# Optimization experiments

Measured on AMD Instinct MI355X. Metric: run time of the kernel, lower is better.

## Reference

```python
import jax, jax.numpy as jnp
import numpy as np

B, L, D, C, DEPTH = 2, 1024, 256, 16, 4
N = L // C  # chunks per sequence
EPS = 1.1920929e-07  # torch RMSNorm default eps = finfo(fp32).eps


def rmsnorm(x, w):
    return x * jax.lax.rsqrt(jnp.mean(x * x, axis=-1, keepdims=True) + EPS) * w


def mlp_apply(ws, x):
    # titans MLP: x @ W0, then silu -> @ W1, ... (works for batched [*,d,d] weights too)
    for i, w in enumerate(ws):
        if i:
            x = jax.nn.silu(x)
        x = x @ w
    return x


def setup_inputs() -> dict:
    key = jax.random.key(0)
    ks = jax.random.split(key, 10)
    s = np.float32(1.0 / np.sqrt(D))
    return {
        "seq": jax.random.normal(ks[0], (B, L, D), jnp.float32),
        "w_store_norm": jnp.ones((D,), jnp.float32),
        "w_retrieve_norm": jnp.ones((D,), jnp.float32),
        "w_post_norm": jnp.ones((D,), jnp.float32),
        "Wq": jax.random.normal(ks[1], (D, D), jnp.float32) * s,
        "Wkv": jax.random.normal(ks[2], (D, 2 * D), jnp.float32) * s,
        "w_adapt": jax.random.normal(ks[3], (D,), jnp.float32) * s,
        "w_mom": jax.random.normal(ks[4], (D,), jnp.float32) * s,
        "w_decay": jax.random.normal(ks[5], (D,), jnp.float32) * s,
        "W0": jax.random.normal(ks[6], (D, D), jnp.float32) * s,
        "W1": jax.random.normal(ks[7], (D, D), jnp.float32) * s,
        "W2": jax.random.normal(ks[8], (D, D), jnp.float32) * s,
        "W3": jax.random.normal(ks[9], (D, D), jnp.float32) * s,
    }


def _forward(seq, w_store_norm, w_retrieve_norm, w_post_norm, Wq, Wkv,
             w_adapt, w_mom, w_decay, W0, W1, W2, W3):
    ws = (W0, W1, W2, W3)

    # ---------------- store_memories ----------------
    sn = rmsnorm(seq, w_store_norm)                      # [B,L,D]; L already multiple of C
    cm = sn.reshape(B, N, C, D).mean(axis=2)             # per-chunk mean [B,N,D]
    adaptive_lr = jax.nn.sigmoid(cm @ w_adapt)           # [B,N]
    adaptive_mom = jax.nn.sigmoid(cm @ w_mom)[..., None]   # [B,N,1]
    decay = jax.nn.sigmoid(cm @ w_decay)[..., None]        # [B,N,1]

    kv = sn @ Wkv                                        # [B,L,2D]
    keys = kv[..., :D].reshape(B * N, C, D)
    vals = kv[..., D:].reshape(B * N, C, D)

    def chunk_loss(params, k, v):
        pred = mlp_apply(params, k)                      # [C,D]
        return jnp.sum(jnp.mean((pred - v) ** 2, axis=-1))

    # per-chunk grads wrt the 4 MLP weights (past weights are zero at init)
    grads = jax.vmap(jax.grad(chunk_loss), in_axes=(None, 0, 0))(ws, keys, vals)
    g = jnp.stack(grads, axis=1).reshape(B, N, DEPTH * D * D)  # packed 'b n *'
    surprise = -adaptive_lr[..., None] * g               # [B,N,P]

    def op(l, r):
        al, xl = l
        ar, xr = r
        return (al * ar, xl * ar + xr)                   # x_t = a_t*x_{t-1} + b_t

    _, momentum = jax.lax.associative_scan(op, (adaptive_mom, surprise), axis=1)
    _, updates = jax.lax.associative_scan(op, (1.0 - decay, momentum), axis=1)
    upd = updates.reshape(B, N, DEPTH, D, D)

    # per-chunk fast weights: base params + cumulative update
    fast_ws = tuple((w + upd[:, :, i]).reshape(B * N, D, D) for i, w in enumerate(ws))

    # ---------------- retrieve_memories ----------------
    rn = rmsnorm(seq, w_retrieve_norm)[:, C - 1:]        # [B, L-C+1, D]
    rn = jnp.pad(rn, ((0, 0), (0, C - 1), (0, 0)))       # pad back up to [B,L,D]
    q = (rn @ Wq).reshape(B * N, C, D)
    out = mlp_apply(fast_ws, q).reshape(B, L, D)         # batched fast-weight MLP
    out = rmsnorm(out, w_post_norm)
    out = jnp.pad(out, ((0, 0), (C - 1, 0), (0, 0)))[:, :-(C - 1)]  # shift by C-1
    return out


def reference(seq, w_store_norm, w_retrieve_norm, w_post_norm, Wq, Wkv,
              w_adapt, w_mom, w_decay, W0, W1, W2, W3):
    return _forward(seq, w_store_norm, w_retrieve_norm, w_post_norm, Wq, Wkv,
                    w_adapt, w_mom, w_decay, W0, W1, W2, W3)
```

## Files before the change

kernel.cpp:

```cpp
#include <hip/hip_runtime.h>
#include <hip/hip_bf16.h>

typedef __attribute__((ext_vector_type(8)))  short s8v;
typedef __attribute__((ext_vector_type(4)))  float f4v;
typedef _Float16 h4 __attribute__((ext_vector_type(4)));
typedef __attribute__((ext_vector_type(4))) unsigned short u4v;

constexpr int NCn  = 128;
constexpr int DDn  = 65536;
constexpr int XP   = 264;
constexpr float EPSf = 1.1920929e-07f;

__device__ __forceinline__ float sigm(float x){ return 1.0f/(1.0f + expf(-x)); }
__device__ __forceinline__ float silu_(float x){ return x * sigm(x); }
__device__ __forceinline__ float dsilu_(float x){ float s = sigm(x); return s*(1.0f + x*(1.0f - s)); }

__device__ __forceinline__ unsigned short f2b(float x){
    __hip_bfloat16 b = __float2bfloat16(x);
    unsigned short u; __builtin_memcpy(&u, &b, 2); return u;
}
__device__ __forceinline__ float b2f(unsigned short u){
    __hip_bfloat16 b; __builtin_memcpy(&b, &u, 2); return __bfloat162float(b);
}
__device__ __forceinline__ h4 ldh4(const unsigned short* p){
    h4 r; __builtin_memcpy(&r, p, 8); return r;
}

__device__ __forceinline__ int fidx(int row, int col){
    return (((row >> 4)*8 + (col >> 5))*4 + ((col >> 3) & 3))*128 + (row & 15)*8 + (col & 7);
}

__global__ __launch_bounds__(256) void ktw(const float* __restrict__ Wq,
        const float* __restrict__ Wkv, const float* __restrict__ W0,
        const float* __restrict__ W1, const float* __restrict__ W2,
        const float* __restrict__ W3, unsigned short* __restrict__ WTb,
        unsigned short* __restrict__ WqTb, unsigned short* __restrict__ WkvTb,
        unsigned short* __restrict__ Wb){
    int z = blockIdx.z;
    if (z >= 6){
        const float* S = (z==6)?W1:(z==7)?W2:W3;
        size_t idx = (((size_t)blockIdx.y*8 + blockIdx.x)*256 + threadIdx.x)*2;
        float2 v = *(const float2*)(S + idx);
        ushort2 u; u.x = f2b(v.x); u.y = f2b(v.y);
        int row = (int)(idx >> 8), col = (int)(idx & 255);
        *(ushort2*)(Wb + (size_t)(z-6)*DDn + fidx(row, col)) = u;
        return;
    }
    __shared__ float tl[32][33];
    if (z != 5 && blockIdx.y >= 8) return;
    const float* S; unsigned short* T; int C;
    if (z < 4){ S = (z==0)?W0:(z==1)?W1:(z==2)?W2:W3; T = WTb + (size_t)z*DDn; C = 256; }
    else if (z == 4){ S = Wq; T = WqTb; C = 256; }
    else { S = Wkv; T = WkvTb; C = 512; }
    int k0 = blockIdx.x*32, j0 = blockIdx.y*32;
    int tx = threadIdx.x & 31, ty = threadIdx.x >> 5;
    #pragma unroll
    for (int p = 0; p < 4; ++p)
        tl[ty + 8*p][tx] = S[(size_t)(k0 + ty + 8*p)*C + j0 + tx];
    __syncthreads();
    #pragma unroll
    for (int p = 0; p < 4; ++p){
        int r = j0 + ty + 8*p, k = k0 + tx;
        T[fidx(r, k)] = f2b(tl[tx][ty + 8*p]);
    }
}

__global__ __launch_bounds__(1024, 1) void kfb(const float* __restrict__ seq,
        const float* __restrict__ wsn,
        const unsigned short* __restrict__ WkvTb, const unsigned short* __restrict__ WTb,
        const unsigned short* __restrict__ Wb,
        const float* __restrict__ wa, const float* __restrict__ wm,
        const float* __restrict__ wdk,
        float* __restrict__ momg, float* __restrict__ decg,
        unsigned short* __restrict__ XT, unsigned short* __restrict__ GT){
    __shared__ unsigned short xs[16][XP];
    __shared__ unsigned short xl[4][16][XP];
    __shared__ unsigned short Gs[16][XP];
    __shared__ float red3[16][4];
    int tid = threadIdx.x, w = tid >> 6, lane = tid & 63;
    int m16 = lane & 15, q16 = lane >> 4;
    int g = blockIdx.x;
    int n0 = w*16;
    size_t fb = (size_t)w*4096 + q16*128 + m16*8;

    {
        const float4 xv = *(const float4*)(seq + ((size_t)g*16 + w)*256 + lane*4);
        const float4 wv = *(const float4*)(wsn + lane*4);
        float ssq = xv.x*xv.x + xv.y*xv.y + xv.z*xv.z + xv.w*xv.w;
        #pragma unroll
        for (int off = 32; off; off >>= 1) ssq += __shfl_xor(ssq, off, 64);
        float s2 = rsqrtf(ssq*(1.f/256.f) + EPSf);
        u4v sv;
        sv[0] = f2b(xv.x*s2*wv.x); sv[1] = f2b(xv.y*s2*wv.y);
        sv[2] = f2b(xv.z*s2*wv.z); sv[3] = f2b(xv.w*s2*wv.w);
        *(u4v*)(&xs[w][lane*4]) = sv;
    }
    __syncthreads();

    float sc;
    {
        int d2 = tid & 255, qt = tid >> 8;
        float a = 0.f;
        #pragma unroll
        for (int c = 0; c < 4; ++c)
            a += b2f(xs[qt*4 + c][d2]);
        float cm = a * (1.f/16.f);
        float s0 = cm*wa[d2], s1 = cm*wm[d2], s2 = cm*wdk[d2];
        #pragma unroll
        for (int off = 32; off; off >>= 1){
            s0 += __shfl_down(s0, off, 64);
            s1 += __shfl_down(s1, off, 64);
            s2 += __shfl_down(s2, off, 64);
        }
        if (lane == 0){ red3[w][0] = s0; red3[w][1] = s1; red3[w][2] = s2; }
        __syncthreads();
        float da = 0.f, dm = 0.f, dc = 0.f;
        #pragma unroll
        for (int i = 0; i < 16; ++i){
            da += red3[i][0]; dm += red3[i][1]; dc += red3[i][2];
        }
        sc = -2.f * sigm(da) * (1.f/256.f);
        if (tid == 0){ momg[g] = sigm(dm); decg[g] = sigm(dc); }
    }

    s8v af[8];
    #pragma unroll
    for (int i = 0; i < 8; ++i) af[i] = *(const s8v*)(&xs[m16][q16*8 + i*32]);

    s8v bpre[8];
    #pragma unroll
    for (int i = 0; i < 8; ++i) bpre[i] = *(const s8v*)(WTb + fb + i*512);

    f4v vacc;
    {
        f4v ka = {0.f,0.f,0.f,0.f}, va = {0.f,0.f,0.f,0.f};
        const unsigned short* brK = WkvTb + fb;
        const unsigned short* brV = WkvTb + (size_t)DDn + fb;
        #pragma unroll
        for (int i = 0; i < 8; ++i){
            s8v bK = *(const s8v*)(brK + i*512);
            s8v bV = *(const s8v*)(brV + i*512);
            ka = __builtin_amdgcn_mfma_f32_16x16x32_bf16(af[i], bK, ka, 0, 0, 0);
            va = __builtin_amdgcn_mfma_f32_16x16x32_bf16(af[i], bV, va, 0, 0, 0);
        }
        vacc = va;
        #pragma unroll
        for (int r = 0; r < 4; ++r) xl[0][4*q16 + r][n0 + m16] = f2b(ka[r]);
    }

    f4v hreg[3];
    #pragma unroll
    for (int l = 0; l < 3; ++l){
        __syncthreads();
        s8v xa[8];
        #pragma unroll
        for (int i = 0; i < 8; ++i)
            xa[i] = *(const s8v*)(&xl[l][m16][q16*8 + i*32]);
        s8v bcur[8];
        #pragma unroll
        for (int i = 0; i < 8; ++i) bcur[i] = bpre[i];
        const unsigned short* nxt = WTb + (size_t)(l+1)*DDn + fb;
        #pragma unroll
        for (int i = 0; i < 8; ++i) bpre[i] = *(const s8v*)(nxt + i*512);
        f4v acc = {0.f,0.f,0.f,0.f};
        #pragma unroll
        for (int i = 0; i < 8; ++i)
            acc = __builtin_amdgcn_mfma_f32_16x16x32_bf16(xa[i], bcur[i], acc, 0, 0, 0);
        hreg[l] = acc;
        #pragma unroll
        for (int r = 0; r < 4; ++r)
            xl[l+1][4*q16 + r][n0 + m16] = f2b(silu_(acc[r]));
    }
    __syncthreads();

    {
        int d = tid & 255, qt = tid >> 8;
        #pragma unroll
        for (int l = 0; l < 4; ++l){
            h4 v;
            #pragma unroll
            for (int j = 0; j < 4; ++j)
                v[j] = (_Float16)b2f(xl[l][qt*4 + j][d]);
            *(h4*)(XT + (((size_t)l*128 + g)*256 + d)*16 + qt*4) = v;
        }
    }

    {
        s8v xa[8];
        #pragma unroll
        for (int i = 0; i < 8; ++i)
            xa[i] = *(const s8v*)(&xl[3][m16][q16*8 + i*32]);
        s8v bcur[8];
        #pragma unroll
        for (int i = 0; i < 8; ++i) bcur[i] = bpre[i];
        const unsigned short* nxt = Wb + (size_t)2*DDn + fb;
        #pragma unroll
        for (int i = 0; i < 8; ++i) bpre[i] = *(const s8v*)(nxt + i*512);
        f4v acc = {0.f,0.f,0.f,0.f};
        #pragma unroll
        for (int i = 0; i < 8; ++i)
            acc = __builtin_amdgcn_mfma_f32_16x16x32_bf16(xa[i], bcur[i], acc, 0, 0, 0);
        #pragma unroll
        for (int r = 0; r < 4; ++r)
            Gs[4*q16 + r][n0 + m16] = f2b(sc * (acc[r] - vacc[r]));
    }
    __syncthreads();
    {
        int d = tid & 255, qt = tid >> 8;
        h4 v;
        #pragma unroll
        for (int j = 0; j < 4; ++j)
            v[j] = (_Float16)b2f(Gs[qt*4 + j][d]);
        *(h4*)(GT + (((size_t)3*128 + g)*256 + d)*16 + qt*4) = v;
    }

    #pragma unroll
    for (int l = 3; l >= 1; --l){
        s8v gfa[8];
        #pragma unroll
        for (int i = 0; i < 8; ++i)
            gfa[i] = *(const s8v*)(&Gs[m16][q16*8 + i*32]);
        s8v bcur[8];
        #pragma unroll
        for (int i = 0; i < 8; ++i) bcur[i] = bpre[i];
        if (l > 1){
            const unsigned short* nxt = Wb + (size_t)(l-2)*DDn + fb;
            #pragma unroll
            for (int i = 0; i < 8; ++i) bpre[i] = *(const s8v*)(nxt + i*512);
        }
        f4v acc = {0.f,0.f,0.f,0.f};
        #pragma unroll
        for (int i = 0; i < 8; ++i)
            acc = __builtin_amdgcn_mfma_f32_16x16x32_bf16(gfa[i], bcur[i], acc, 0, 0, 0);
        f4v gn;
        #pragma unroll
        for (int r = 0; r < 4; ++r)
            gn[r] = acc[r] * dsilu_(hreg[l-1][r]);
        __syncthreads();
        #pragma unroll
        for (int r = 0; r < 4; ++r)
            Gs[4*q16 + r][n0 + m16] = f2b(gn[r]);
        __syncthreads();
        {
            int d = tid & 255, qt = tid >> 8;
            h4 v;
            #pragma unroll
            for (int j = 0; j < 4; ++j)
                v[j] = (_Float16)b2f(Gs[qt*4 + j][d]);
            *(h4*)(GT + (((size_t)(l-1)*128 + g)*256 + d)*16 + qt*4) = v;
        }
    }
}

__global__ __launch_bounds__(64, 1) void kck(const unsigned short* __restrict__ XT,
        const unsigned short* __restrict__ GT, const float* __restrict__ momg,
        const float* __restrict__ decg, unsigned short* __restrict__ ucpb){
    __shared__ unsigned short ts[16][18];
    int lane = threadIdx.x;
    int m16 = lane & 15, q16 = lane >> 4;
    int rt = blockIdx.x, ct = blockIdx.y, bl = blockIdx.z;
    int b = bl >> 2, l = bl & 3;
    int dr = rt*16 + m16;
    const unsigned short* Gb = GT + ((size_t)l*128 + b*64)*4096 + (size_t)dr*16 + q16*4;
    const unsigned short* X0 = XT + ((size_t)l*128 + b*64)*4096
                             + (size_t)(ct*16 + m16)*16 + q16*4;
    int rr = lane & 15, cg = lane >> 4;
    int off0;
    {
        int c0 = ct*16 + cg*4;
        off0 = ((rt*8 + (c0 >> 5))*4 + ((c0 >> 3) & 3))*128 + rr*8 + (c0 & 7);
    }
    f4v us = {0.f,0.f,0.f,0.f}, ms = {0.f,0.f,0.f,0.f};
    #pragma unroll 4
    for (int n = 0; n < 64; ++n){
        float mo = momg[b*64 + n], de = 1.f - decg[b*64 + n];
        h4 a  = ldh4(Gb + (size_t)n*4096);
        h4 x0 = ldh4(X0 + (size_t)n*4096);
        f4v z = {0.f,0.f,0.f,0.f};
        f4v s = __builtin_amdgcn_mfma_f32_16x16x16f16(a, x0, z, 0, 0, 0);
        #pragma unroll
        for (int r = 0; r < 4; ++r){
            float mn = mo*ms[r] + s[r], un = de*us[r] + mn;
            ms[r] = mn; us[r] = un;
            ts[4*q16 + r][m16] = f2b(un);
        }
        size_t cb = ((size_t)bl*64 + n)*65536;
        u4v v0;
        #pragma unroll
        for (int j = 0; j < 4; ++j)
            v0[j] = ts[rr][cg*4 + j];
        *(u4v*)(ucpb + cb + off0) = v0;
    }
}

__global__ __launch_bounds__(1024, 1) void kretr(const float* __restrict__ seq,
        const float* __restrict__ wrn,
        const unsigned short* __restrict__ WqTb, const unsigned short* __restrict__ WTb,
        const unsigned short* __restrict__ ucpb, const float* __restrict__ wpost,
        float* __restrict__ out){
    __shared__ unsigned short xc[2][16][XP];
    __shared__ float red[16][16];
    __shared__ float rs[16];
    int tid = threadIdx.x, w = tid >> 6, lane = tid & 63;
    int m16 = lane & 15, q16 = lane >> 4;
    int g = blockIdx.x;
    int b = g >> 6, nl = g & 63;
    int n0 = w*16;
    size_t fb = (size_t)w*4096 + q16*128 + m16*8;
    const unsigned short* ubase = ucpb + ((size_t)(b*4)*64 + nl)*65536 + fb;

    s8v upre[8];
    #pragma unroll
    for (int i = 0; i < 8; ++i) upre[i] = *(const s8v*)(ubase + i*512);

    {
        int p = nl*16 + w + 15;
        u4v sv = {0,0,0,0};
        if (p < 1024){
            const float4 xv = *(const float4*)(seq + ((size_t)b*1024 + p)*256 + lane*4);
            const float4 wv = *(const float4*)(wrn + lane*4);
            float ssq = xv.x*xv.x + xv.y*xv.y + xv.z*xv.z + xv.w*xv.w;
            #pragma unroll
            for (int off = 32; off; off >>= 1) ssq += __shfl_xor(ssq, off, 64);
            float s2 = rsqrtf(ssq*(1.f/256.f) + EPSf);
            sv[0] = f2b(xv.x*s2*wv.x); sv[1] = f2b(xv.y*s2*wv.y);
            sv[2] = f2b(xv.z*s2*wv.z); sv[3] = f2b(xv.w*s2*wv.w);
        }
        *(u4v*)(&xc[1][w][lane*4]) = sv;
    }
    __syncthreads();

    {
        s8v a[8];
        #pragma unroll
        for (int i = 0; i < 8; ++i) a[i] = *(const s8v*)(&xc[1][m16][q16*8 + i*32]);
        f4v acc = {0.f,0.f,0.f,0.f};
        const unsigned short* br = WqTb + fb;
        #pragma unroll
        for (int i = 0; i < 8; ++i){
            s8v bb = *(const s8v*)(br + i*512);
            acc = __builtin_amdgcn_mfma_f32_16x16x32_bf16(a[i], bb, acc, 0, 0, 0);
        }
        #pragma unroll
        for (int r = 0; r < 4; ++r) xc[0][4*q16 + r][n0 + m16] = f2b(acc[r]);
    }
    __syncthreads();

    f4v hacc;
    for (int l = 0; l < 4; ++l){
        s8v xa[8];
        #pragma unroll
        for (int i = 0; i < 8; ++i)
            xa[i] = *(const s8v*)(&xc[l & 1][m16][q16*8 + i*32]);
        s8v ucur[8];
        #pragma unroll
        for (int i = 0; i < 8; ++i) ucur[i] = upre[i];
        if (l < 3){
            const unsigned short* un = ubase + (size_t)(l+1)*64*65536;
            #pragma unroll
            for (int i = 0; i < 8; ++i) upre[i] = *(const s8v*)(un + i*512);
        }
        const unsigned short* br = WTb + (size_t)l*DDn + fb;
        f4v aW = {0.f,0.f,0.f,0.f}, aU = {0.f,0.f,0.f,0.f};
        #pragma unroll
        for (int i = 0; i < 8; ++i){
            s8v w0 = *(const s8v*)(br + i*512);
            aW = __builtin_amdgcn_mfma_f32_16x16x32_bf16(xa[i], w0, aW, 0, 0, 0);
            aU = __builtin_amdgcn_mfma_f32_16x16x32_bf16(xa[i], ucur[i], aU, 0, 0, 0);
        }
        #pragma unroll
        for (int r = 0; r < 4; ++r) hacc[r] = aW[r] + aU[r];
        if (l < 3){
            #pragma unroll
            for (int r = 0; r < 4; ++r)
                xc[(l + 1) & 1][4*q16 + r][n0 + m16] = f2b(silu_(hacc[r]));
            __syncthreads();
        }
    }

    float part[4];
    #pragma unroll
    for (int r = 0; r < 4; ++r) part[r] = hacc[r]*hacc[r];
    #pragma unroll
    for (int off = 1; off < 16; off <<= 1)
        #pragma unroll
        for (int r = 0; r < 4; ++r) part[r] += __shfl_xor(part[r], off, 64);
    if (m16 == 0)
        #pragma unroll
        for (int r = 0; r < 4; ++r) red[w][4*q16 + r] = part[r];
    __syncthreads();
    if (tid < 16){
        float s = 0.f;
        #pragma unroll
        for (int i = 0; i < 16; ++i) s += red[i][tid];
        rs[tid] = rsqrtf(s*(1.f/256.f) + EPSf);
    }
    __syncthreads();
    {
        int d = n0 + m16;
        float wp = wpost[d];
        #pragma unroll
        for (int r = 0; r < 4; ++r){
            int c = 4*q16 + r;
            int tp = nl*16 + c + 15;
            if (tp < 1024)
                out[((size_t)b*1024 + tp)*256 + d] = hacc[r]*rs[c]*wp;
        }
    }
    if (nl == 0){
        for (int idx = tid; idx < 15*256; idx += 1024)
            out[(size_t)b*262144 + idx] = 0.f;
    }
}

extern "C" void kernel_launch(void* const* d_in, const int* in_sizes, int n_in,
                              void* d_out, int out_size, void* d_ws, size_t ws_size,
                              hipStream_t stream) {
    const float* seq     = (const float*)d_in[0];
    const float* w_store = (const float*)d_in[1];
    const float* w_retr  = (const float*)d_in[2];
    const float* w_post  = (const float*)d_in[3];
    const float* Wq      = (const float*)d_in[4];
    const float* Wkv     = (const float*)d_in[5];
    const float* w_adapt = (const float*)d_in[6];
    const float* w_mom   = (const float*)d_in[7];
    const float* w_decay = (const float*)d_in[8];
    const float* W0      = (const float*)d_in[9];
    const float* W1      = (const float*)d_in[10];
    const float* W2      = (const float*)d_in[11];
    const float* W3      = (const float*)d_in[12];

    float* momg  = (float*)d_ws;
    float* decg  = momg + NCn;
    unsigned short* WTb   = (unsigned short*)(decg + NCn + 32);
    unsigned short* Wb    = WTb   + 4*(size_t)DDn;
    unsigned short* WqTb  = Wb    + 3*(size_t)DDn;
    unsigned short* WkvTb = WqTb  + (size_t)DDn;
    unsigned short* XT    = WkvTb + 2*(size_t)DDn;
    unsigned short* GT    = XT    + (size_t)4*NCn*4096;
    unsigned short* ucpb  = GT    + (size_t)4*NCn*4096;

    ktw   <<<dim3(8, 16, 9),  256,  0, stream>>>(Wq, Wkv, W0, W1, W2, W3,
                                                 WTb, WqTb, WkvTb, Wb);
    kfb   <<<dim3(NCn),       1024, 0, stream>>>(seq, w_store, WkvTb, WTb, Wb,
                                                 w_adapt, w_mom, w_decay,
                                                 momg, decg, XT, GT);
    kck   <<<dim3(16, 16, 8), 64,   0, stream>>>(XT, GT, momg, decg, ucpb);
    kretr <<<dim3(NCn),       1024, 0, stream>>>(seq, w_retr, WqTb, WTb, ucpb,
                                                 w_post, (float*)d_out);
}
```

Before: 138.1 us.

## Fuse forward, chunk-scan and retrieval kernels into one cooperative kernel

Merges the three kernels kfb, kck and kretr into a single cooperative kernel with 128 blocks of 1024 threads, separated by grid-wide syncs. The scan phase is remapped so that each of the 16 waves per block handles one of the former 64-thread kck blocks. This removes two kernel launch boundaries and their inter-kernel gaps. In exchange it adds the cost of grid barriers and the cooperative-launch overhead, and it places all the phases' shared memory in one block, which could limit scheduling.

```diff
diff --git a/kernel.cpp b/kernel.cpp
--- a/kernel.cpp
+++ b/kernel.cpp
@@ -1,5 +1,8 @@
 #include <hip/hip_runtime.h>
 #include <hip/hip_bf16.h>
+#include <hip/hip_cooperative_groups.h>
+
+namespace cg = cooperative_groups;
 
 typedef __attribute__((ext_vector_type(8)))  short s8v;
 typedef __attribute__((ext_vector_type(4)))  float f4v;
@@ -65,18 +68,25 @@
     }
 }
 
-__global__ __launch_bounds__(1024, 1) void kfb(const float* __restrict__ seq,
-        const float* __restrict__ wsn,
+__global__ __launch_bounds__(1024, 1) void kmain(const float* __restrict__ seq,
+        const float* __restrict__ wsn, const float* __restrict__ wrn,
         const unsigned short* __restrict__ WkvTb, const unsigned short* __restrict__ WTb,
-        const unsigned short* __restrict__ Wb,
+        const unsigned short* __restrict__ Wb, const unsigned short* __restrict__ WqTb,
         const float* __restrict__ wa, const float* __restrict__ wm,
         const float* __restrict__ wdk,
         float* __restrict__ momg, float* __restrict__ decg,
-        unsigned short* __restrict__ XT, unsigned short* __restrict__ GT){
+        unsigned short* __restrict__ XT, unsigned short* __restrict__ GT,
+        unsigned short* __restrict__ ucpb,
+        const float* __restrict__ wpost, float* __restrict__ out){
     __shared__ unsigned short xs[16][XP];
     __shared__ unsigned short xl[4][16][XP];
     __shared__ unsigned short Gs[16][XP];
     __shared__ float red3[16][4];
+    __shared__ unsigned short ts[16][16][18];
+    __shared__ unsigned short xc[2][16][XP];
+    __shared__ float red[16][16];
+    __shared__ float rs[16];
+
     int tid = threadIdx.x, w = tid >> 6, lane = tid & 63;
     int m16 = lane & 15, q16 = lane >> 4;
     int g = blockIdx.x;
@@ -84,162 +94,127 @@
     size_t fb = (size_t)w*4096 + q16*128 + m16*8;
 
     {
-        const float4 xv = *(const float4*)(seq + ((size_t)g*16 + w)*256 + lane*4);
-        const float4 wv = *(const float4*)(wsn + lane*4);
-        float ssq = xv.x*xv.x + xv.y*xv.y + xv.z*xv.z + xv.w*xv.w;
-        #pragma unroll
-        for (int off = 32; off; off >>= 1) ssq += __shfl_xor(ssq, off, 64);
-        float s2 = rsqrtf(ssq*(1.f/256.f) + EPSf);
-        u4v sv;
-        sv[0] = f2b(xv.x*s2*wv.x); sv[1] = f2b(xv.y*s2*wv.y);
-        sv[2] = f2b(xv.z*s2*wv.z); sv[3] = f2b(xv.w*s2*wv.w);
-        *(u4v*)(&xs[w][lane*4]) = sv;
-    }
-    __syncthreads();
-
-    float sc;
-    {
-        int d2 = tid & 255, qt = tid >> 8;
-        float a = 0.f;
-        #pragma unroll
-        for (int c = 0; c < 4; ++c)
-            a += b2f(xs[qt*4 + c][d2]);
-        float cm = a * (1.f/16.f);
-        float s0 = cm*wa[d2], s1 = cm*wm[d2], s2 = cm*wdk[d2];
-        #pragma unroll
-        for (int off = 32; off; off >>= 1){
-            s0 += __shfl_down(s0, off, 64);
-            s1 += __shfl_down(s1, off, 64);
-            s2 += __shfl_down(s2, off, 64);
-        }
-        if (lane == 0){ red3[w][0] = s0; red3[w][1] = s1; red3[w][2] = s2; }
-        __syncthreads();
-        float da = 0.f, dm = 0.f, dc = 0.f;
-        #pragma unroll
-        for (int i = 0; i < 16; ++i){
-            da += red3[i][0]; dm += red3[i][1]; dc += red3[i][2];
-        }
-        sc = -2.f * sigm(da) * (1.f/256.f);
-        if (tid == 0){ momg[g] = sigm(dm); decg[g] = sigm(dc); }
-    }
-
-    s8v af[8];
-    #pragma unroll
-    for (int i = 0; i < 8; ++i) af[i] = *(const s8v*)(&xs[m16][q16*8 + i*32]);
-
-    s8v bpre[8];
-    #pragma unroll
-    for (int i = 0; i < 8; ++i) bpre[i] = *(const s8v*)(WTb + fb + i*512);
-
-    f4v vacc;
-    {
-        f4v ka = {0.f,0.f,0.f,0.f}, va = {0.f,0.f,0.f,0.f};
-        const unsigned short* brK = WkvTb + fb;
-        const unsigned short* brV = WkvTb + (size_t)DDn + fb;
-        #pragma unroll
-        for (int i = 0; i < 8; ++i){
-            s8v bK = *(const s8v*)(brK + i*512);
-            s8v bV = *(const s8v*)(brV + i*512);
-            ka = __builtin_amdgcn_mfma_f32_16x16x32_bf16(af[i], bK, ka, 0, 0, 0);
-            va = __builtin_amdgcn_mfma_f32_16x16x32_bf16(af[i], bV, va, 0, 0, 0);
-        }
-        vacc = va;
-        #pragma unroll
-        for (int r = 0; r < 4; ++r) xl[0][4*q16 + r][n0 + m16] = f2b(ka[r]);
-    }
-
-    f4v hreg[3];
-    #pragma unroll
-    for (int l = 0; l < 3; ++l){
-        __syncthreads();
-        s8v xa[8];
-        #pragma unroll
-        for (int i = 0; i < 8; ++i)
-            xa[i] = *(const s8v*)(&xl[l][m16][q16*8 + i*32]);
-        s8v bcur[8];
-        #pragma unroll
-        for (int i = 0; i < 8; ++i) bcur[i] = bpre[i];
-        const unsigned short* nxt = WTb + (size_t)(l+1)*DDn + fb;
-        #pragma unroll
-        for (int i = 0; i < 8; ++i) bpre[i] = *(const s8v*)(nxt + i*512);
-        f4v acc = {0.f,0.f,0.f,0.f};
-        #pragma unroll
-        for (int i = 0; i < 8; ++i)
-            acc = __builtin_amdgcn_mfma_f32_16x16x32_bf16(xa[i], bcur[i], acc, 0, 0, 0);
-        hreg[l] = acc;
-        #pragma unroll
-        for (int r = 0; r < 4; ++r)
-            xl[l+1][4*q16 + r][n0 + m16] = f2b(silu_(acc[r]));
-    }
-    __syncthreads();
-
-    {
-        int d = tid & 255, qt = tid >> 8;
-        #pragma unroll
-        for (int l = 0; l < 4; ++l){
-            h4 v;
-            #pragma unroll
-            for (int j = 0; j < 4; ++j)
-                v[j] = (_Float16)b2f(xl[l][qt*4 + j][d]);
-            *(h4*)(XT + (((size_t)l*128 + g)*256 + d)*16 + qt*4) = v;
-        }
-    }
-
-    {
-        s8v xa[8];
-        #pragma unroll
-        for (int i = 0; i < 8; ++i)
-            xa[i] = *(const s8v*)(&xl[3][m16][q16*8 + i*32]);
-        s8v bcur[8];
-        #pragma unroll
-        for (int i = 0; i < 8; ++i) bcur[i] = bpre[i];
-        const unsigned short* nxt = Wb + (size_t)2*DDn + fb;
-        #pragma unroll
-        for (int i = 0; i < 8; ++i) bpre[i] = *(const s8v*)(nxt + i*512);
-        f4v acc = {0.f,0.f,0.f,0.f};
-        #pragma unroll
-        for (int i = 0; i < 8; ++i)
-            acc = __builtin_amdgcn_mfma_f32_16x16x32_bf16(xa[i], bcur[i], acc, 0, 0, 0);
-        #pragma unroll
-        for (int r = 0; r < 4; ++r)
-            Gs[4*q16 + r][n0 + m16] = f2b(sc * (acc[r] - vacc[r]));
-    }
-    __syncthreads();
-    {
-        int d = tid & 255, qt = tid >> 8;
-        h4 v;
-        #pragma unroll
-        for (int j = 0; j < 4; ++j)
-            v[j] = (_Float16)b2f(Gs[qt*4 + j][d]);
-        *(h4*)(GT + (((size_t)3*128 + g)*256 + d)*16 + qt*4) = v;
-    }
-
-    #pragma unroll
-    for (int l = 3; l >= 1; --l){
-        s8v gfa[8];
-        #pragma unroll
-        for (int i = 0; i < 8; ++i)
-            gfa[i] = *(const s8v*)(&Gs[m16][q16*8 + i*32]);
-        s8v bcur[8];
-        #pragma unroll
-        for (int i = 0; i < 8; ++i) bcur[i] = bpre[i];
-        if (l > 1){
-            const unsigned short* nxt = Wb + (size_t)(l-2)*DDn + fb;
+        {
+            const float4 xv = *(const float4*)(seq + ((size_t)g*16 + w)*256 + lane*4);
+            const float4 wv = *(const float4*)(wsn + lane*4);
+            float ssq = xv.x*xv.x + xv.y*xv.y + xv.z*xv.z + xv.w*xv.w;
+            #pragma unroll
+            for (int off = 32; off; off >>= 1) ssq += __shfl_xor(ssq, off, 64);
+            float s2 = rsqrtf(ssq*(1.f/256.f) + EPSf);
+            u4v sv;
+            sv[0] = f2b(xv.x*s2*wv.x); sv[1] = f2b(xv.y*s2*wv.y);
+            sv[2] = f2b(xv.z*s2*wv.z); sv[3] = f2b(xv.w*s2*wv.w);
+            *(u4v*)(&xs[w][lane*4]) = sv;
+        }
+        __syncthreads();
+
+        float sc;
+        {
+            int d2 = tid & 255, qt = tid >> 8;
+            float a = 0.f;
+            #pragma unroll
+            for (int c = 0; c < 4; ++c)
+                a += b2f(xs[qt*4 + c][d2]);
+            float cm = a * (1.f/16.f);
+            float s0 = cm*wa[d2], s1 = cm*wm[d2], s2 = cm*wdk[d2];
+            #pragma unroll
+            for (int off = 32; off; off >>= 1){
+                s0 += __shfl_down(s0, off, 64);
+                s1 += __shfl_down(s1, off, 64);
+                s2 += __shfl_down(s2, off, 64);
+            }
+            if (lane == 0){ red3[w][0] = s0; red3[w][1] = s1; red3[w][2] = s2; }
+            __syncthreads();
+            float da = 0.f, dm = 0.f, dc = 0.f;
+            #pragma unroll
+            for (int i = 0; i < 16; ++i){
+                da += red3[i][0]; dm += red3[i][1]; dc += red3[i][2];
+            }
+            sc = -2.f * sigm(da) * (1.f/256.f);
+            if (tid == 0){ momg[g] = sigm(dm); decg[g] = sigm(dc); }
+        }
+
+        s8v af[8];
+        #pragma unroll
+        for (int i = 0; i < 8; ++i) af[i] = *(const s8v*)(&xs[m16][q16*8 + i*32]);
+
+        s8v bpre[8];
+        #pragma unroll
+        for (int i = 0; i < 8; ++i) bpre[i] = *(const s8v*)(WTb + fb + i*512);
+
+        f4v vacc;
+        {
+            f4v ka = {0.f,0.f,0.f,0.f}, va = {0.f,0.f,0.f,0.f};
+            const unsigned short* brK = WkvTb + fb;
+            const unsigned short* brV = WkvTb + (size_t)DDn + fb;
+            #pragma unroll
+            for (int i = 0; i < 8; ++i){
+                s8v bK = *(const s8v*)(brK + i*512);
+                s8v bV = *(const s8v*)(brV + i*512);
+                ka = __builtin_amdgcn_mfma_f32_16x16x32_bf16(af[i], bK, ka, 0, 0, 0);
+                va = __builtin_amdgcn_mfma_f32_16x16x32_bf16(af[i], bV, va, 0, 0, 0);
+            }
+            vacc = va;
+            #pragma unroll
+            for (int r = 0; r < 4; ++r) xl[0][4*q16 + r][n0 + m16] = f2b(ka[r]);
+        }
+
+        f4v hreg[3];
+        #pragma unroll
+        for (int l = 0; l < 3; ++l){
+            __syncthreads();
+            s8v xa[8];
+            #pragma unroll
+            for (int i = 0; i < 8; ++i)
+                xa[i] = *(const s8v*)(&xl[l][m16][q16*8 + i*32]);
+            s8v bcur[8];
+            #pragma unroll
+            for (int i = 0; i < 8; ++i) bcur[i] = bpre[i];
+            const unsigned short* nxt = WTb + (size_t)(l+1)*DDn + fb;
             #pragma unroll
             for (int i = 0; i < 8; ++i) bpre[i] = *(const s8v*)(nxt + i*512);
-        }
-        f4v acc = {0.f,0.f,0.f,0.f};
-        #pragma unroll
-        for (int i = 0; i < 8; ++i)
-            acc = __builtin_amdgcn_mfma_f32_16x16x32_bf16(gfa[i], bcur[i], acc, 0, 0, 0);
-        f4v gn;
-        #pragma unroll
-        for (int r = 0; r < 4; ++r)
-            gn[r] = acc[r] * dsilu_(hreg[l-1][r]);
-        __syncthreads();
-        #pragma unroll
-        for (int r = 0; r < 4; ++r)
-            Gs[4*q16 + r][n0 + m16] = f2b(gn[r]);
+            f4v acc = {0.f,0.f,0.f,0.f};
+            #pragma unroll
+            for (int i = 0; i < 8; ++i)
+                acc = __builtin_amdgcn_mfma_f32_16x16x32_bf16(xa[i], bcur[i], acc, 0, 0, 0);
+            hreg[l] = acc;
+            #pragma unroll
+            for (int r = 0; r < 4; ++r)
+                xl[l+1][4*q16 + r][n0 + m16] = f2b(silu_(acc[r]));
+        }
+        __syncthreads();
+
+        {
+            int d = tid & 255, qt = tid >> 8;
+            #pragma unroll
+            for (int l = 0; l < 4; ++l){
+                h4 v;
+                #pragma unroll
+                for (int j = 0; j < 4; ++j)
+                    v[j] = (_Float16)b2f(xl[l][qt*4 + j][d]);
+                *(h4*)(XT + (((size_t)l*128 + g)*256 + d)*16 + qt*4) = v;
+            }
+        }
+
+        {
+            s8v xa[8];
+            #pragma unroll
+            for (int i = 0; i < 8; ++i)
+                xa[i] = *(const s8v*)(&xl[3][m16][q16*8 + i*32]);
+            s8v bcur[8];
+            #pragma unroll
+            for (int i = 0; i < 8; ++i) bcur[i] = bpre[i];
+            const unsigned short* nxt = Wb + (size_t)2*DDn + fb;
+            #pragma unroll
+            for (int i = 0; i < 8; ++i) bpre[i] = *(const s8v*)(nxt + i*512);
+            f4v acc = {0.f,0.f,0.f,0.f};
+            #pragma unroll
+            for (int i = 0; i < 8; ++i)
+                acc = __builtin_amdgcn_mfma_f32_16x16x32_bf16(xa[i], bcur[i], acc, 0, 0, 0);
+            #pragma unroll
+            for (int r = 0; r < 4; ++r)
+                Gs[4*q16 + r][n0 + m16] = f2b(sc * (acc[r] - vacc[r]));
+        }
         __syncthreads();
         {
             int d = tid & 255, qt = tid >> 8;
@@ -247,169 +222,194 @@
             #pragma unroll
             for (int j = 0; j < 4; ++j)
                 v[j] = (_Float16)b2f(Gs[qt*4 + j][d]);
-            *(h4*)(GT + (((size_t)(l-1)*128 + g)*256 + d)*16 + qt*4) = v;
+            *(h4*)(GT + (((size_t)3*128 + g)*256 + d)*16 + qt*4) = v;
+        }
+
+        #pragma unroll
+        for (int l = 3; l >= 1; --l){
+            s8v gfa[8];
+            #pragma unroll
+            for (int i = 0; i < 8; ++i)
+                gfa[i] = *(const s8v*)(&Gs[m16][q16*8 + i*32]);
+            s8v bcur[8];
+            #pragma unroll
+            for (int i = 0; i < 8; ++i) bcur[i] = bpre[i];
+            if (l > 1){
+                const unsigned short* nxt = Wb + (size_t)(l-2)*DDn + fb;
+                #pragma unroll
+                for (int i = 0; i < 8; ++i) bpre[i] = *(const s8v*)(nxt + i*512);
+            }
+            f4v acc = {0.f,0.f,0.f,0.f};
+            #pragma unroll
+            for (int i = 0; i < 8; ++i)
+                acc = __builtin_amdgcn_mfma_f32_16x16x32_bf16(gfa[i], bcur[i], acc, 0, 0, 0);
+            f4v gn;
+            #pragma unroll
+            for (int r = 0; r < 4; ++r)
+                gn[r] = acc[r] * dsilu_(hreg[l-1][r]);
+            __syncthreads();
+            #pragma unroll
+            for (int r = 0; r < 4; ++r)
+                Gs[4*q16 + r][n0 + m16] = f2b(gn[r]);
+            __syncthreads();
+            {
+                int d = tid & 255, qt = tid >> 8;
+                h4 v;
+                #pragma unroll
+                for (int j = 0; j < 4; ++j)
+                    v[j] = (_Float16)b2f(Gs[qt*4 + j][d]);
+                *(h4*)(GT + (((size_t)(l-1)*128 + g)*256 + d)*16 + qt*4) = v;
+            }
         }
     }
-}
-
-__global__ __launch_bounds__(64, 1) void kck(const unsigned short* __restrict__ XT,
-        const unsigned short* __restrict__ GT, const float* __restrict__ momg,
-        const float* __restrict__ decg, unsigned short* __restrict__ ucpb){
-    __shared__ unsigned short ts[16][18];
-    int lane = threadIdx.x;
-    int m16 = lane & 15, q16 = lane >> 4;
-    int rt = blockIdx.x, ct = blockIdx.y, bl = blockIdx.z;
-    int b = bl >> 2, l = bl & 3;
-    int dr = rt*16 + m16;
-    const unsigned short* Gb = GT + ((size_t)l*128 + b*64)*4096 + (size_t)dr*16 + q16*4;
-    const unsigned short* X0 = XT + ((size_t)l*128 + b*64)*4096
-                             + (size_t)(ct*16 + m16)*16 + q16*4;
-    int rr = lane & 15, cg = lane >> 4;
-    int off0;
+
+    cg::this_grid().sync();
+
     {
-        int c0 = ct*16 + cg*4;
-        off0 = ((rt*8 + (c0 >> 5))*4 + ((c0 >> 3) & 3))*128 + rr*8 + (c0 & 7);
+        int W = g*16 + w;
+        int rt = W >> 7, ct = (W >> 3) & 15, bl = W & 7;
+        int b = bl >> 2, l = bl & 3;
+        int dr = rt*16 + m16;
+        const unsigned short* Gb = GT + ((size_t)l*128 + b*64)*4096 + (size_t)dr*16 + q16*4;
+        const unsigned short* X0 = XT + ((size_t)l*128 + b*64)*4096
+                                 + (size_t)(ct*16 + m16)*16 + q16*4;
+        int rr = lane & 15, cg2 = lane >> 4;
+        int off0;
+        {
+            int c0 = ct*16 + cg2*4;
+            off0 = ((rt*8 + (c0 >> 5))*4 + ((c0 >> 3) & 3))*128 + rr*8 + (c0 & 7);
+        }
+        f4v us = {0.f,0.f,0.f,0.f}, ms = {0.f,0.f,0.f,0.f};
+        #pragma unroll 4
+        for (int n = 0; n < 64; ++n){
+            float mo = momg[b*64 + n], de = 1.f - decg[b*64 + n];
+            h4 a  = ldh4(Gb + (size_t)n*4096);
+            h4 x0 = ldh4(X0 + (size_t)n*4096);
+            f4v z = {0.f,0.f,0.f,0.f};
+            f4v s = __builtin_amdgcn_mfma_f32_16x16x16f16(a, x0, z, 0, 0, 0);
+            #pragma unroll
+            for (int r = 0; r < 4; ++r){
+                float mn = mo*ms[r] + s[r], un = de*us[r] + mn;
+                ms[r] = mn; us[r] = un;
+                ts[w][4*q16 + r][m16] = f2b(un);
+            }
+            size_t cb = ((size_t)bl*64 + n)*65536;
+            u4v v0;
+            #pragma unroll
+            for (int j = 0; j < 4; ++j)
+                v0[j] = ts[w][rr][cg2*4 + j];
+            *(u4v*)(ucpb + cb + off0) = v0;
+        }
     }
-    f4v us = {0.f,0.f,0.f,0.f}, ms = {0.f,0.f,0.f,0.f};
-    #pragma unroll 4
-    for (int n = 0; n < 64; ++n){
-        float mo = momg[b*64 + n], de = 1.f - decg[b*64 + n];
-        h4 a  = ldh4(Gb + (size_t)n*4096);
-        h4 x0 = ldh4(X0 + (size_t)n*4096);
-        f4v z = {0.f,0.f,0.f,0.f};
-        f4v s = __builtin_amdgcn_mfma_f32_16x16x16f16(a, x0, z, 0, 0, 0);
-        #pragma unroll
-        for (int r = 0; r < 4; ++r){
-            float mn = mo*ms[r] + s[r], un = de*us[r] + mn;
-            ms[r] = mn; us[r] = un;
-            ts[4*q16 + r][m16] = f2b(un);
-        }
-        size_t cb = ((size_t)bl*64 + n)*65536;
-        u4v v0;
-        #pragma unroll
-        for (int j = 0; j < 4; ++j)
-            v0[j] = ts[rr][cg*4 + j];
-        *(u4v*)(ucpb + cb + off0) = v0;
-    }
-}
-
-__global__ __launch_bounds__(1024, 1) void kretr(const float* __restrict__ seq,
-        const float* __restrict__ wrn,
-        const unsigned short* __restrict__ WqTb, const unsigned short* __restrict__ WTb,
-        const unsigned short* __restrict__ ucpb, const float* __restrict__ wpost,
-        float* __restrict__ out){
-    __shared__ unsigned short xc[2][16][XP];
-    __shared__ float red[16][16];
-    __shared__ float rs[16];
-    int tid = threadIdx.x, w = tid >> 6, lane = tid & 63;
-    int m16 = lane & 15, q16 = lane >> 4;
-    int g = blockIdx.x;
-    int b = g >> 6, nl = g & 63;
-    int n0 = w*16;
-    size_t fb = (size_t)w*4096 + q16*128 + m16*8;
-    const unsigned short* ubase = ucpb + ((size_t)(b*4)*64 + nl)*65536 + fb;
-
-    s8v upre[8];
-    #pragma unroll
-    for (int i = 0; i < 8; ++i) upre[i] = *(const s8v*)(ubase + i*512);
+
+    cg::this_grid().sync();
 
     {
-        int p = nl*16 + w + 15;
-        u4v sv = {0,0,0,0};
-        if (p < 1024){
-            const float4 xv = *(const float4*)(seq + ((size_t)b*1024 + p)*256 + lane*4);
-            const float4 wv = *(const float4*)(wrn + lane*4);
-            float ssq = xv.x*xv.x + xv.y*xv.y + xv.z*xv.z + xv.w*xv.w;
-            #pragma unroll
-            for (int off = 32; off; off >>= 1) ssq += __shfl_xor(ssq, off, 64);
-            float s2 = rsqrtf(ssq*(1.f/256.f) + EPSf);
-            sv[0] = f2b(xv.x*s2*wv.x); sv[1] = f2b(xv.y*s2*wv.y);
-            sv[2] = f2b(xv.z*s2*wv.z); sv[3] = f2b(xv.w*s2*wv.w);
-        }
-        *(u4v*)(&xc[1][w][lane*4]) = sv;
-    }
-    __syncthreads();
-
-    {
-        s8v a[8];
-        #pragma unroll
-        for (int i = 0; i < 8; ++i) a[i] = *(const s8v*)(&xc[1][m16][q16*8 + i*32]);
-        f4v acc = {0.f,0.f,0.f,0.f};
-        const unsigned short* br = WqTb + fb;
-        #pragma unroll
-        for (int i = 0; i < 8; ++i){
-            s8v bb = *(const s8v*)(br + i*512);
-            acc = __builtin_amdgcn_mfma_f32_16x16x32_bf16(a[i], bb, acc, 0, 0, 0);
-        }
-        #pragma unroll
-        for (int r = 0; r < 4; ++r) xc[0][4*q16 + r][n0 + m16] = f2b(acc[r]);
-    }
-    __syncthreads();
-
-    f4v hacc;
-    for (int l = 0; l < 4; ++l){
-        s8v xa[8];
-        #pragma unroll
-        for (int i = 0; i < 8; ++i)
-            xa[i] = *(const s8v*)(&xc[l & 1][m16][q16*8 + i*32]);
-        s8v ucur[8];
-        #pragma unroll
-        for (int i = 0; i < 8; ++i) ucur[i] = upre[i];
-        if (l < 3){
-            const unsigned short* un = ubase + (size_t)(l+1)*64*65536;
-            #pragma unroll
-            for (int i = 0; i < 8; ++i) upre[i] = *(const s8v*)(un + i*512);
-        }
-        const unsigned short* br = WTb + (size_t)l*DDn + fb;
-        f4v aW = {0.f,0.f,0.f,0.f}, aU = {0.f,0.f,0.f,0.f};
-        #pragma unroll
-        for (int i = 0; i < 8; ++i){
-            s8v w0 = *(const s8v*)(br + i*512);
-            aW = __builtin_amdgcn_mfma_f32_16x16x32_bf16(xa[i], w0, aW, 0, 0, 0);
-            aU = __builtin_amdgcn_mfma_f32_16x16x32_bf16(xa[i], ucur[i], aU, 0, 0, 0);
-        }
-        #pragma unroll
-        for (int r = 0; r < 4; ++r) hacc[r] = aW[r] + aU[r];
-        if (l < 3){
-            #pragma unroll
-            for (int r = 0; r < 4; ++r)
-                xc[(l + 1) & 1][4*q16 + r][n0 + m16] = f2b(silu_(hacc[r]));
-            __syncthreads();
-        }
-    }
-
-    float part[4];
-    #pragma unroll
-    for (int r = 0; r < 4; ++r) part[r] = hacc[r]*hacc[r];
-    #pragma unroll
-    for (int off = 1; off < 16; off <<= 1)
-        #pragma unroll
-        for (int r = 0; r < 4; ++r) part[r] += __shfl_xor(part[r], off, 64);
-    if (m16 == 0)
-        #pragma unroll
-        for (int r = 0; r < 4; ++r) red[w][4*q16 + r] = part[r];
-    __syncthreads();
-    if (tid < 16){
-        float s = 0.f;
-        #pragma unroll
-        for (int i = 0; i < 16; ++i) s += red[i][tid];
-        rs[tid] = rsqrtf(s*(1.f/256.f) + EPSf);
-    }
-    __syncthreads();
-    {
-        int d = n0 + m16;
-        float wp = wpost[d];
-        #pragma unroll
-        for (int r = 0; r < 4; ++r){
-            int c = 4*q16 + r;
-            int tp = nl*16 + c + 15;
-            if (tp < 1024)
-                out[((size_t)b*1024 + tp)*256 + d] = hacc[r]*rs[c]*wp;
-        }
-    }
-    if (nl == 0){
-        for (int idx = tid; idx < 15*256; idx += 1024)
-            out[(size_t)b*262144 + idx] = 0.f;
+        int b = g >> 6, nl = g & 63;
+        const unsigned short* ubase = ucpb + ((size_t)(b*4)*64 + nl)*65536 + fb;
+
+        s8v upre[8];
+        #pragma unroll
+        for (int i = 0; i < 8; ++i) upre[i] = *(const s8v*)(ubase + i*512);
+
+        {
+            int p = nl*16 + w + 15;
+            u4v sv = {0,0,0,0};
+            if (p < 1024){
+                const float4 xv = *(const float4*)(seq + ((size_t)b*1024 + p)*256 + lane*4);
+                const float4 wv = *(const float4*)(wrn + lane*4);
+                float ssq = xv.x*xv.x + xv.y*xv.y + xv.z*xv.z + xv.w*xv.w;
+                #pragma unroll
+                for (int off = 32; off; off >>= 1) ssq += __shfl_xor(ssq, off, 64);
+                float s2 = rsqrtf(ssq*(1.f/256.f) + EPSf);
+                sv[0] = f2b(xv.x*s2*wv.x); sv[1] = f2b(xv.y*s2*wv.y);
+                sv[2] = f2b(xv.z*s2*wv.z); sv[3] = f2b(xv.w*s2*wv.w);
+            }
+            *(u4v*)(&xc[1][w][lane*4]) = sv;
+        }
+        __syncthreads();
+
+        {
+            s8v a[8];
+            #pragma unroll
+            for (int i = 0; i < 8; ++i) a[i] = *(const s8v*)(&xc[1][m16][q16*8 + i*32]);
+            f4v acc = {0.f,0.f,0.f,0.f};
+            const unsigned short* br = WqTb + fb;
+            #pragma unroll
+            for (int i = 0; i < 8; ++i){
+                s8v bb = *(const s8v*)(br + i*512);
+                acc = __builtin_amdgcn_mfma_f32_16x16x32_bf16(a[i], bb, acc, 0, 0, 0);
+            }
+            #pragma unroll
+            for (int r = 0; r < 4; ++r) xc[0][4*q16 + r][n0 + m16] = f2b(acc[r]);
+        }
+        __syncthreads();
+
+        f4v hacc;
+        for (int l = 0; l < 4; ++l){
+            s8v xa[8];
+            #pragma unroll
+            for (int i = 0; i < 8; ++i)
+                xa[i] = *(const s8v*)(&xc[l & 1][m16][q16*8 + i*32]);
+            s8v ucur[8];
+            #pragma unroll
+            for (int i = 0; i < 8; ++i) ucur[i] = upre[i];
+            if (l < 3){
+                const unsigned short* un = ubase + (size_t)(l+1)*64*65536;
+                #pragma unroll
+                for (int i = 0; i < 8; ++i) upre[i] = *(const s8v*)(un + i*512);
+            }
+            const unsigned short* br = WTb + (size_t)l*DDn + fb;
+            f4v aW = {0.f,0.f,0.f,0.f}, aU = {0.f,0.f,0.f,0.f};
+            #pragma unroll
+            for (int i = 0; i < 8; ++i){
+                s8v w0 = *(const s8v*)(br + i*512);
+                aW = __builtin_amdgcn_mfma_f32_16x16x32_bf16(xa[i], w0, aW, 0, 0, 0);
+                aU = __builtin_amdgcn_mfma_f32_16x16x32_bf16(xa[i], ucur[i], aU, 0, 0, 0);
+            }
+            #pragma unroll
+            for (int r = 0; r < 4; ++r) hacc[r] = aW[r] + aU[r];
+            if (l < 3){
+                #pragma unroll
+                for (int r = 0; r < 4; ++r)
+                    xc[(l + 1) & 1][4*q16 + r][n0 + m16] = f2b(silu_(hacc[r]));
+                __syncthreads();
+            }
+        }
+
+        float part[4];
+        #pragma unroll
+        for (int r = 0; r < 4; ++r) part[r] = hacc[r]*hacc[r];
+        #pragma unroll
+        for (int off = 1; off < 16; off <<= 1)
+            #pragma unroll
+            for (int r = 0; r < 4; ++r) part[r] += __shfl_xor(part[r], off, 64);
+        if (m16 == 0)
+            #pragma unroll
+            for (int r = 0; r < 4; ++r) red[w][4*q16 + r] = part[r];
+        __syncthreads();
+        if (tid < 16){
+            float s = 0.f;
+            #pragma unroll
+            for (int i = 0; i < 16; ++i) s += red[i][tid];
+            rs[tid] = rsqrtf(s*(1.f/256.f) + EPSf);
+        }
+        __syncthreads();
+        {
+            int d = n0 + m16;
+            float wp = wpost[d];
+            #pragma unroll
+            for (int r = 0; r < 4; ++r){
+                int c = 4*q16 + r;
+                int tp = nl*16 + c + 15;
+                if (tp < 1024)
+                    out[((size_t)b*1024 + tp)*256 + d] = hacc[r]*rs[c]*wp;
+            }
+        }
+        if (nl == 0){
+            for (int idx = tid; idx < 15*256; idx += 1024)
+                out[(size_t)b*262144 + idx] = 0.f;
+        }
     }
 }
 
@@ -439,13 +439,17 @@
     unsigned short* XT    = WkvTb + 2*(size_t)DDn;
     unsigned short* GT    = XT    + (size_t)4*NCn*4096;
     unsigned short* ucpb  = GT    + (size_t)4*NCn*4096;
-
-    ktw   <<<dim3(8, 16, 9),  256,  0, stream>>>(Wq, Wkv, W0, W1, W2, W3,
-                                                 WTb, WqTb, WkvTb, Wb);
-    kfb   <<<dim3(NCn),       1024, 0, stream>>>(seq, w_store, WkvTb, WTb, Wb,
-                                                 w_adapt, w_mom, w_decay,
-                                                 momg, decg, XT, GT);
-    kck   <<<dim3(16, 16, 8), 64,   0, stream>>>(XT, GT, momg, decg, ucpb);
-    kretr <<<dim3(NCn),       1024, 0, stream>>>(seq, w_retr, WqTb, WTb, ucpb,
-                                                 w_post, (float*)d_out);
-}
+    float* outp = (float*)d_out;
+
+    ktw <<<dim3(8, 16, 9), 256, 0, stream>>>(Wq, Wkv, W0, W1, W2, W3,
+                                             WTb, WqTb, WkvTb, Wb);
+
+    void* args[] = { (void*)&seq, (void*)&w_store, (void*)&w_retr,
+                     (void*)&WkvTb, (void*)&WTb, (void*)&Wb, (void*)&WqTb,
+                     (void*)&w_adapt, (void*)&w_mom, (void*)&w_decay,
+                     (void*)&momg, (void*)&decg,
+                     (void*)&XT, (void*)&GT, (void*)&ucpb,
+                     (void*)&w_post, (void*)&outp };
+    hipLaunchCooperativeKernel((void*)kmain, dim3(NCn), dim3(1024),
+                               args, 0, stream);
+}
```

Measured after the change: 207.7 us. 1.5x slower.
